# Kernel optimization log

Hardware: AMD Instinct MI355X
Metric: run time of the kernel (lower is better)

## Reference

```python
import jax, jax.numpy as jnp
import numpy as np

N_A = 50000
N_B = 50000
E = 800000
C_IN = 128
C_OUT = 128


def _lstm_cell_seq1(x, W_ih, b):
    # PyTorch LSTM with seq_len=1 and zero initial state: h = o*tanh(i*g)
    # gate order in weight_ih: [i, f, g, o]; f-gate is unused since c0 = 0.
    gates = x @ W_ih.T + b  # [N, 4H]
    i, f, g, o = jnp.split(gates, 4, axis=-1)
    c = jax.nn.sigmoid(i) * jnp.tanh(g)
    return jax.nn.sigmoid(o) * jnp.tanh(c)


def _conv(x_src, x_dst, edge_index, W_ih, b_lstm, W_lin, b_lin):
    # LSTM message depends only on src features -> compute per node, gather per edge.
    msg = _lstm_cell_seq1(x_src, W_ih, b_lstm)          # [N_src, C_OUT]
    src, dst = edge_index[0], edge_index[1]
    aggr = jax.ops.segment_sum(msg[src], dst, num_segments=x_dst.shape[0])  # [N_dst, C_OUT]
    h = jnp.concatenate([x_dst, aggr], axis=-1)          # [N_dst, C_IN + C_OUT]
    return jax.nn.relu(h @ W_lin.T + b_lin)              # dropout = identity (eval mode)


def setup_inputs() -> dict:
    key = jax.random.key(0)
    ks = jax.random.split(key, 12)
    s = 0.05
    return {
        "x_a": jax.random.normal(ks[0], (N_A, C_IN), jnp.float32),
        "x_b": jax.random.normal(ks[1], (N_B, C_IN), jnp.float32),
        "edge_ab": jax.random.randint(ks[2], (2, E), 0, 50000, jnp.int64 if jax.config.jax_enable_x64 else jnp.int32),
        "edge_ba": jax.random.randint(ks[3], (2, E), 0, 50000, jnp.int64 if jax.config.jax_enable_x64 else jnp.int32),
        "W_ih_ab": jax.random.normal(ks[4], (4 * C_OUT, C_IN), jnp.float32) * s,
        "b_ab": jax.random.normal(ks[5], (4 * C_OUT,), jnp.float32) * s,
        "W_lin_ab": jax.random.normal(ks[6], (C_OUT, C_IN + C_OUT), jnp.float32) * s,
        "b_lin_ab": jax.random.normal(ks[7], (C_OUT,), jnp.float32) * s,
        "W_ih_ba": jax.random.normal(ks[8], (4 * C_OUT, C_IN), jnp.float32) * s,
        "b_ba": jax.random.normal(ks[9], (4 * C_OUT,), jnp.float32) * s,
        "W_lin_ba": jax.random.normal(ks[10], (C_OUT, C_IN + C_OUT), jnp.float32) * s,
        "b_lin_ba": jax.random.normal(ks[11], (C_OUT,), jnp.float32) * s,
    }


def reference(x_a, x_b, edge_ab, edge_ba,
              W_ih_ab, b_ab, W_lin_ab, b_lin_ab,
              W_ih_ba, b_ba, W_lin_ba, b_lin_ba):
    # a_to_b relation updates type_b nodes; b_to_a updates type_a nodes.
    out_b = _conv(x_a, x_b, edge_ab, W_ih_ab, b_ab, W_lin_ab, b_lin_ab)
    out_a = _conv(x_b, x_a, edge_ba, W_ih_ba, b_ba, W_lin_ba, b_lin_ba)
    # stack (same shapes) => [2, N, C_OUT]: index 0 = new x_a, index 1 = new x_b
    return jnp.stack([out_a, out_b], axis=0)
```

## Files before the change

kernel.cpp:

```cpp
#include <hip/hip_runtime.h>
#include <cstdint>
#include <cstddef>

#define CCH 128
#define TK 4096
#define FCAP 2560
#define SLOT 2560
#define MAXBKT 1024
#define XPAD 136
#define APAD 264

typedef __attribute__((ext_vector_type(8))) short short8;
typedef __attribute__((ext_vector_type(4))) float floatx4;

__device__ __forceinline__ unsigned short f2bf(float f) {
    unsigned u = __builtin_bit_cast(unsigned, f);
    u += 0x7fffu + ((u >> 16) & 1u);
    return (unsigned short)(u >> 16);
}
__device__ __forceinline__ float bf2f(unsigned short h) {
    unsigned u = ((unsigned)h) << 16;
    return __builtin_bit_cast(float, u);
}
__device__ __forceinline__ float sigmoidf_(float x) { return 1.0f / (1.0f + __expf(-x)); }
__device__ __forceinline__ float tanh_fast(float x) {
    x = fminf(fmaxf(x, -10.0f), 10.0f);
    float e = __expf(2.0f * x);
    return (e - 1.0f) / (e + 1.0f);
}

__global__ __launch_bounds__(256) void prep_weights_kernel(
    const float* __restrict__ Wih0, const float* __restrict__ Wih1,
    const float* __restrict__ Wlin0, const float* __restrict__ Wlin1,
    unsigned short* __restrict__ frag_ih, unsigned short* __restrict__ frag_lin,
    int* __restrict__ btot, int NBKT)
{
    int t = blockIdx.x * 256 + threadIdx.x;
    if (t < 12288) {
        int l  = t & 63;
        int kc = (t >> 6) & 3;
        int ct = (t >> 8) & 7;
        int g  = (t >> 11) % 3;
        int rel = t / 6144;
        int gb = (g == 0) ? 0 : (g == 1 ? 256 : 384);
        const float* W = rel ? Wih1 : Wih0;
        int n  = gb + ct * 16 + (l & 15);
        int kb = kc * 32 + (l >> 4) * 8;
        unsigned short* o = frag_ih + (size_t)t * 8;
#pragma unroll
        for (int j = 0; j < 8; j++) o[j] = f2bf(W[(size_t)n * CCH + kb + j]);
    } else if (t < 20480) {
        int t2 = t - 12288;
        int l  = t2 & 63;
        int kc = (t2 >> 6) & 7;
        int ct = (t2 >> 9) & 7;
        int rel = t2 >> 12;
        const float* W = rel ? Wlin1 : Wlin0;
        int n  = ct * 16 + (l & 15);
        int kb = kc * 32 + (l >> 4) * 8;
        unsigned short* o = frag_lin + (size_t)t2 * 8;
#pragma unroll
        for (int j = 0; j < 8; j++) o[j] = f2bf(W[(size_t)n * 256 + kb + j]);
    } else {
        int z = t - 20480;
        if (z < NBKT) btot[z] = 0;
    }
}

__global__ __launch_bounds__(256) void lstm_scatter_kernel(
    const float* __restrict__ x0, const float* __restrict__ x1,
    const unsigned short* __restrict__ wfrag,
    const float* __restrict__ b0, const float* __restrict__ b1,
    unsigned short* __restrict__ msg0, unsigned short* __restrict__ msg1,
    int N0, int N1, int nblk0,
    const int* __restrict__ src0, const int* __restrict__ dst0,
    const int* __restrict__ src1, const int* __restrict__ dst1,
    int* __restrict__ btot, unsigned* __restrict__ packed,
    int E0, int E1, int nbkt0, int NBKT, int nT)
{
    __shared__ unsigned short xs[32 * XPAD];
    __shared__ int h[MAXBKT];
    __shared__ int cur[MAXBKT];
    const int tid = threadIdx.x;

    if (blockIdx.x < nT) {
        for (int i = tid; i < NBKT; i += 256) h[i] = 0;
        __syncthreads();
        const long long Etot = (long long)E0 + E1;
        const long long base = (long long)blockIdx.x * TK;
        int gg[16];
        unsigned pk[16];
#pragma unroll
        for (int j = 0; j < 16; j++) {
            long long e = base + j * 256 + tid;
            gg[j] = -1;
            if (e < Etot) {
                int s, d, g;
                if (e < E0) { d = dst0[e]; s = src0[e]; g = d >> 7; }
                else { long long ee = e - E0; d = dst1[ee]; s = src1[ee]; g = nbkt0 + (d >> 7); }
                gg[j] = g;
                pk[j] = ((unsigned)(d & 127) << 24) | (unsigned)s;
                atomicAdd(&h[g], 1);
            }
        }
        __syncthreads();
        for (int i = tid; i < NBKT; i += 256) {
            int c = h[i];
            cur[i] = i * SLOT + (c ? atomicAdd(&btot[i], c) : 0);
        }
        __syncthreads();
#pragma unroll
        for (int j = 0; j < 16; j++) {
            if (gg[j] >= 0) {
                int pos = atomicAdd(&cur[gg[j]], 1);
                packed[pos] = pk[j];
            }
        }
        return;
    }

    const int lb = blockIdx.x - nT;
    const int rel = (lb >= nblk0);
    const int nb = (rel ? (lb - nblk0) : lb) * 32;
    const float* x = rel ? x1 : x0;
    const float* bias = rel ? b1 : b0;
    unsigned short* msg = rel ? msg1 : msg0;
    const int N = rel ? N1 : N0;
    const unsigned short* wf = wfrag + (size_t)rel * 6144 * 8;

    {
        int r = tid >> 3;
        int c0 = (tid & 7) * 16;
        int n = nb + r;
        unsigned short* dstp = xs + r * XPAD + c0;
        if (n < N) {
            const float4* srcp = (const float4*)(x + (size_t)n * CCH + c0);
#pragma unroll
            for (int qq = 0; qq < 4; qq++) {
                float4 v = srcp[qq];
                unsigned u0 = (unsigned)f2bf(v.x) | ((unsigned)f2bf(v.y) << 16);
                unsigned u1 = (unsigned)f2bf(v.z) | ((unsigned)f2bf(v.w) << 16);
                *(uint2*)(dstp + qq * 4) = make_uint2(u0, u1);
            }
        } else {
#pragma unroll
            for (int qq = 0; qq < 4; qq++) *(uint2*)(dstp + qq * 4) = make_uint2(0u, 0u);
        }
    }
    __syncthreads();

    const int w = tid >> 6;
    const int l = tid & 63;
    const int ctb2 = w * 2;
    const int q = l >> 4;
    const int m16 = l & 15;

    floatx4 acc[3][2][2];
#pragma unroll
    for (int g = 0; g < 3; g++)
#pragma unroll
        for (int c = 0; c < 2; c++)
#pragma unroll
            for (int mt = 0; mt < 2; mt++) acc[g][c][mt] = (floatx4){0.f, 0.f, 0.f, 0.f};

    const unsigned short* arow0 = xs + m16 * XPAD + q * 8;
    const unsigned short* arow1 = xs + (16 + m16) * XPAD + q * 8;
#pragma unroll
    for (int kc = 0; kc < 4; kc++) {
        short8 af0 = *(const short8*)(arow0 + kc * 32);
        short8 af1 = *(const short8*)(arow1 + kc * 32);
#pragma unroll
        for (int g = 0; g < 3; g++)
#pragma unroll
            for (int c = 0; c < 2; c++) {
                const unsigned short* bp = wf + ((((size_t)g * 8 + (ctb2 + c)) * 4 + kc) * 64 + l) * 8;
                short8 bv = *(const short8*)bp;
                acc[g][c][0] = __builtin_amdgcn_mfma_f32_16x16x32_bf16(af0, bv, acc[g][c][0], 0, 0, 0);
                acc[g][c][1] = __builtin_amdgcn_mfma_f32_16x16x32_bf16(af1, bv, acc[g][c][1], 0, 0, 0);
            }
    }

    __syncthreads();
#pragma unroll
    for (int c = 0; c < 2; c++) {
        const int col = (ctb2 + c) * 16 + m16;
        const float bi = bias[col], bg = bias[256 + col], bo = bias[384 + col];
#pragma unroll
        for (int mt = 0; mt < 2; mt++)
#pragma unroll
            for (int r = 0; r < 4; r++) {
                const int nl = mt * 16 + q * 4 + r;
                float iv = sigmoidf_(acc[0][c][mt][r] + bi);
                float gv = tanh_fast(acc[1][c][mt][r] + bg);
                float ov = sigmoidf_(acc[2][c][mt][r] + bo);
                xs[nl * XPAD + col] = f2bf(ov * tanh_fast(iv * gv));
            }
    }
    __syncthreads();
    {
        int r = tid >> 3;
        int c0 = (tid & 7) * 16;
        int n = nb + r;
        if (n < N) {
            const unsigned short* srow = xs + r * XPAD + c0;
            uint4 v0 = *(const uint4*)(srow);
            uint4 v1 = *(const uint4*)(srow + 8);
            unsigned short* drow = msg + (size_t)n * CCH + c0;
            *(uint4*)(drow) = v0;
            *(uint4*)(drow + 8) = v1;
        }
    }
}

__global__ __launch_bounds__(512) void fine_sort_kernel(
    unsigned* __restrict__ packed, const int* __restrict__ btot,
    int* __restrict__ offs0, int* __restrict__ deg0,
    int* __restrict__ offs1, int* __restrict__ deg1,
    int N0, int N1, int nbkt0)
{
    __shared__ unsigned pin[FCAP];
    __shared__ int hist[128], scn[128], cur[128];
    const int g = blockIdx.x;
    const int tid = threadIdx.x;
    const int base = g * SLOT;
    const int cnt = min(btot[g], FCAP);

    for (int i = tid; i < cnt; i += 512) pin[i] = packed[base + i];
    if (tid < 128) hist[tid] = 0;
    __syncthreads();
    for (int i = tid; i < cnt; i += 512) atomicAdd(&hist[pin[i] >> 24], 1);
    __syncthreads();
    int v = (tid < 128) ? hist[tid] : 0;
    if (tid < 128) scn[tid] = v;
    __syncthreads();
    for (int off = 1; off < 128; off <<= 1) {
        int t = (tid >= off && tid < 128) ? scn[tid - off] : 0;
        __syncthreads();
        if (tid < 128) scn[tid] += t;
        __syncthreads();
    }
    if (tid < 128) {
        int excl = scn[tid] - v;
        cur[tid] = excl;
        const int rel = (g >= nbkt0);
        const int lb = rel ? g - nbkt0 : g;
        const int n = lb * 128 + tid;
        const int N = rel ? N1 : N0;
        if (n < N) {
            if (rel) { offs1[n] = base + excl; deg1[n] = v; }
            else     { offs0[n] = base + excl; deg0[n] = v; }
        }
    }
    __syncthreads();
    int* op = (int*)packed;
    for (int i = tid; i < cnt; i += 512) {
        unsigned p = pin[i];
        int pos = atomicAdd(&cur[p >> 24], 1);
        op[base + pos] = (int)(p & 0x00FFFFFFu);
    }
}

__global__ __launch_bounds__(512) void gather_linear_kernel(
    const float* __restrict__ xd0, const float* __restrict__ xd1,
    const unsigned short* __restrict__ msg0, const unsigned short* __restrict__ msg1,
    const int* __restrict__ csr,
    const int* __restrict__ offs0, const int* __restrict__ offs1,
    const int* __restrict__ deg0, const int* __restrict__ deg1,
    const unsigned short* __restrict__ wfrag,
    const float* __restrict__ bl0, const float* __restrict__ bl1,
    float* __restrict__ out0, float* __restrict__ out1,
    int P0, int P1, int N0, int N1)
{
    __shared__ unsigned short s[32 * APAD];
    const int tid = threadIdx.x;
    const int grp = blockIdx.x >> 3;
    const int sub = blockIdx.x & 7;
    const int rel = (sub >> 2) & 1;
    const int lb = grp * 4 + (sub & 3);
    const int P = rel ? P1 : P0;
    if (lb >= P) return;
    const int nb = lb * 32;
    const float* xd = rel ? xd1 : xd0;
    const unsigned short* msg = rel ? msg1 : msg0;
    const int* offs = rel ? offs1 : offs0;
    const int* deg = rel ? deg1 : deg0;
    const float* bl = rel ? bl1 : bl0;
    float* outp = rel ? out1 : out0;
    const int N = rel ? N1 : N0;
    const unsigned short* wf = wfrag + (size_t)rel * 4096 * 8;

    {
        int r = tid >> 4;
        int c0 = (tid & 15) * 8;
        int n = nb + r;
        unsigned short* drow = s + r * APAD + c0;
        if (n < N) {
            const floatx4* srcp = (const floatx4*)(xd + (size_t)n * CCH + c0);
            floatx4 v0 = __builtin_nontemporal_load(srcp);
            floatx4 v1 = __builtin_nontemporal_load(srcp + 1);
            uint4 u;
            u.x = (unsigned)f2bf(v0[0]) | ((unsigned)f2bf(v0[1]) << 16);
            u.y = (unsigned)f2bf(v0[2]) | ((unsigned)f2bf(v0[3]) << 16);
            u.z = (unsigned)f2bf(v1[0]) | ((unsigned)f2bf(v1[1]) << 16);
            u.w = (unsigned)f2bf(v1[2]) | ((unsigned)f2bf(v1[3]) << 16);
            *(uint4*)drow = u;
        } else {
            *(uint4*)drow = make_uint4(0u, 0u, 0u, 0u);
        }
    }
    {
        const int w = tid >> 6;
        const int l = tid & 63;
        const int g = l >> 4;
        const int c = l & 15;
        const int nloc = w * 4 + g;
        const int n = nb + nloc;
        float a0 = 0.f, a1 = 0.f, a2 = 0.f, a3 = 0.f;
        float a4 = 0.f, a5 = 0.f, a6 = 0.f, a7 = 0.f;
        if (n < N) {
            const int start = offs[n];
            const int cnt = deg[n];
            const int* ce = csr + start;
            const unsigned short* mb = msg + c * 8;
#define ACC8(U) { \
            a0 += bf2f((unsigned short)(U.x)); a1 += bf2f((unsigned short)((U.x) >> 16)); \
            a2 += bf2f((unsigned short)(U.y)); a3 += bf2f((unsigned short)((U.y) >> 16)); \
            a4 += bf2f((unsigned short)(U.z)); a5 += bf2f((unsigned short)((U.z) >> 16)); \
            a6 += bf2f((unsigned short)(U.w)); a7 += bf2f((unsigned short)((U.w) >> 16)); }
            int j = 0;
            if (cnt >= 4) {
                int s0 = ce[0], s1 = ce[1], s2 = ce[2], s3 = ce[3];
                for (; j + 8 <= cnt; j += 4) {
                    uint4 u0 = *(const uint4*)(mb + (size_t)s0 * CCH);
                    uint4 u1 = *(const uint4*)(mb + (size_t)s1 * CCH);
                    uint4 u2 = *(const uint4*)(mb + (size_t)s2 * CCH);
                    uint4 u3 = *(const uint4*)(mb + (size_t)s3 * CCH);
                    s0 = ce[j + 4]; s1 = ce[j + 5]; s2 = ce[j + 6]; s3 = ce[j + 7];
                    ACC8(u0); ACC8(u1); ACC8(u2); ACC8(u3);
                }
                uint4 u0 = *(const uint4*)(mb + (size_t)s0 * CCH);
                uint4 u1 = *(const uint4*)(mb + (size_t)s1 * CCH);
                uint4 u2 = *(const uint4*)(mb + (size_t)s2 * CCH);
                uint4 u3 = *(const uint4*)(mb + (size_t)s3 * CCH);
                ACC8(u0); ACC8(u1); ACC8(u2); ACC8(u3);
                j += 4;
            }
            for (; j < cnt; j++) {
                uint4 u0 = *(const uint4*)(mb + (size_t)ce[j] * CCH);
                ACC8(u0);
            }
#undef ACC8
        }
        uint4 o;
        o.x = (unsigned)f2bf(a0) | ((unsigned)f2bf(a1) << 16);
        o.y = (unsigned)f2bf(a2) | ((unsigned)f2bf(a3) << 16);
        o.z = (unsigned)f2bf(a4) | ((unsigned)f2bf(a5) << 16);
        o.w = (unsigned)f2bf(a6) | ((unsigned)f2bf(a7) << 16);
        *(uint4*)(s + nloc * APAD + CCH + c * 8) = o;
    }
    __syncthreads();

    const int w = tid >> 6;
    const int l = tid & 63;
    const int q = l >> 4;
    const int m16 = l & 15;

    floatx4 acc[2];
    acc[0] = (floatx4){0.f, 0.f, 0.f, 0.f};
    acc[1] = (floatx4){0.f, 0.f, 0.f, 0.f};

    const unsigned short* arow0 = s + m16 * APAD + q * 8;
    const unsigned short* arow1 = s + (16 + m16) * APAD + q * 8;
#pragma unroll
    for (int kc = 0; kc < 8; kc++) {
        short8 af0 = *(const short8*)(arow0 + kc * 32);
        short8 af1 = *(const short8*)(arow1 + kc * 32);
        const unsigned short* bp = wf + ((((size_t)w) * 8 + kc) * 64 + l) * 8;
        short8 bv = *(const short8*)bp;
        acc[0] = __builtin_amdgcn_mfma_f32_16x16x32_bf16(af0, bv, acc[0], 0, 0, 0);
        acc[1] = __builtin_amdgcn_mfma_f32_16x16x32_bf16(af1, bv, acc[1], 0, 0, 0);
    }

    const int col = w * 16 + m16;
    const float bv = bl[col];
#pragma unroll
    for (int mt = 0; mt < 2; mt++)
#pragma unroll
        for (int r = 0; r < 4; r++) {
            const int node = nb + mt * 16 + q * 4 + r;
            if (node < N) {
                float v = fmaxf(acc[mt][r] + bv, 0.0f);
                __builtin_nontemporal_store(v, &outp[(size_t)node * CCH + col]);
            }
        }
}

extern "C" void kernel_launch(void* const* d_in, const int* in_sizes, int n_in,
                              void* d_out, int out_size, void* d_ws, size_t ws_size,
                              hipStream_t stream) {
    const float* x_a      = (const float*)d_in[0];
    const float* x_b      = (const float*)d_in[1];
    const int*   e_ab     = (const int*)d_in[2];
    const int*   e_ba     = (const int*)d_in[3];
    const float* W_ih_ab  = (const float*)d_in[4];
    const float* b_ab     = (const float*)d_in[5];
    const float* W_lin_ab = (const float*)d_in[6];
    const float* b_lin_ab = (const float*)d_in[7];
    const float* W_ih_ba  = (const float*)d_in[8];
    const float* b_ba     = (const float*)d_in[9];
    const float* W_lin_ba = (const float*)d_in[10];
    const float* b_lin_ba = (const float*)d_in[11];

    const int NA = in_sizes[0] / CCH;
    const int NB = in_sizes[1] / CCH;
    const int E0 = in_sizes[2] / 2;
    const int E1 = in_sizes[3] / 2;

    float* out = (float*)d_out;
    char* ws = (char*)d_ws;
    size_t off = 0;
    auto alloc = [&](size_t bytes) { char* p = ws + off; off += (bytes + 255) & ~(size_t)255; return p; };

    unsigned short* wfrag_ih  = (unsigned short*)alloc(12288 * 8 * 2);
    unsigned short* wfrag_lin = (unsigned short*)alloc(8192 * 8 * 2);
    unsigned short* msg_a     = (unsigned short*)alloc((size_t)NA * CCH * 2);
    unsigned short* msg_b     = (unsigned short*)alloc((size_t)NB * CCH * 2);

    const int nbkt0 = (NB + 127) / 128;
    const int nbkt1 = (NA + 127) / 128;
    const int NBKT = nbkt0 + nbkt1;
    const long long Etot = (long long)E0 + E1;
    const int nT = (int)((Etot + TK - 1) / TK);

    int* btot   = (int*)alloc((size_t)NBKT * 4);
    int* offs_b = (int*)alloc((size_t)NB * 4);
    int* offs_a = (int*)alloc((size_t)NA * 4);
    int* deg_b  = (int*)alloc((size_t)NB * 4);
    int* deg_a  = (int*)alloc((size_t)NA * 4);
    unsigned* packed = (unsigned*)alloc((size_t)(NBKT + 1) * SLOT * 4);

    const int nblkA = (NA + 31) / 32;
    const int nblkB = (NB + 31) / 32;

    const int prepG = 80 + (NBKT + 255) / 256;
    prep_weights_kernel<<<prepG, 256, 0, stream>>>(
        W_ih_ab, W_ih_ba, W_lin_ab, W_lin_ba, wfrag_ih, wfrag_lin, btot, NBKT);

    lstm_scatter_kernel<<<nT + nblkA + nblkB, 256, 0, stream>>>(
        x_a, x_b, wfrag_ih, b_ab, b_ba, msg_a, msg_b, NA, NB, nblkA,
        e_ab, e_ab + E0, e_ba, e_ba + E1, btot, packed, E0, E1, nbkt0, NBKT, nT);

    fine_sort_kernel<<<NBKT, 512, 0, stream>>>(
        packed, btot, offs_b, deg_b, offs_a, deg_a, NB, NA, nbkt0);

    const int Pmax = (nblkB > nblkA) ? nblkB : nblkA;
    const int G = ((Pmax + 3) / 4) * 8;
    gather_linear_kernel<<<G, 512, 0, stream>>>(
        x_b, x_a, msg_a, msg_b, (const int*)packed,
        offs_b, offs_a, deg_b, deg_a, wfrag_lin, b_lin_ab, b_lin_ba,
        out + (size_t)NA * CCH, out, nblkB, nblkA, NB, NA);
}
```

Measured before the change: 235.9 us.

## Fuse bucket fine-sort into gather-linear kernel using shared-memory CSR

Merges the per-bucket fine sort and the gather+linear kernels into one kernel: each block sorts its 128-node bucket into shared memory and then processes four 32-node tiles, reading neighbour lists from LDS instead of global CSR/offset/degree arrays. This removes a kernel launch and the global round trip of the sorted CSR and offset/degree arrays. In exchange, each block uses much more LDS (about 37 KB), which lowers occupancy. The grid also drops to roughly 782 large blocks that run four serialized gather/MFMA phases, which reduces parallelism and latency hiding for the random gathers.

```diff
diff --git a/kernel.cpp b/kernel.cpp
--- a/kernel.cpp
+++ b/kernel.cpp
@@ -212,187 +212,159 @@
     }
 }
 
-__global__ __launch_bounds__(512) void fine_sort_kernel(
-    unsigned* __restrict__ packed, const int* __restrict__ btot,
-    int* __restrict__ offs0, int* __restrict__ deg0,
-    int* __restrict__ offs1, int* __restrict__ deg1,
+__global__ __launch_bounds__(512) void sort_gather_linear_kernel(
+    const float* __restrict__ xd0, const float* __restrict__ xd1,
+    const unsigned short* __restrict__ msg0, const unsigned short* __restrict__ msg1,
+    const unsigned* __restrict__ packed, const int* __restrict__ btot,
+    const unsigned short* __restrict__ wfrag,
+    const float* __restrict__ bl0, const float* __restrict__ bl1,
+    float* __restrict__ out0, float* __restrict__ out1,
     int N0, int N1, int nbkt0)
 {
     __shared__ unsigned pin[FCAP];
-    __shared__ int hist[128], scn[128], cur[128];
+    __shared__ int sout_s[FCAP];
+    __shared__ int hist[128], scn[128], cur[128], ndoff[128];
+    __shared__ unsigned short s[32 * APAD];
+
+    const int tid = threadIdx.x;
     const int g = blockIdx.x;
-    const int tid = threadIdx.x;
-    const int base = g * SLOT;
-    const int cnt = min(btot[g], FCAP);
-
-    for (int i = tid; i < cnt; i += 512) pin[i] = packed[base + i];
-    if (tid < 128) hist[tid] = 0;
-    __syncthreads();
-    for (int i = tid; i < cnt; i += 512) atomicAdd(&hist[pin[i] >> 24], 1);
-    __syncthreads();
-    int v = (tid < 128) ? hist[tid] : 0;
-    if (tid < 128) scn[tid] = v;
-    __syncthreads();
-    for (int off = 1; off < 128; off <<= 1) {
-        int t = (tid >= off && tid < 128) ? scn[tid - off] : 0;
-        __syncthreads();
-        if (tid < 128) scn[tid] += t;
-        __syncthreads();
-    }
-    if (tid < 128) {
-        int excl = scn[tid] - v;
-        cur[tid] = excl;
-        const int rel = (g >= nbkt0);
-        const int lb = rel ? g - nbkt0 : g;
-        const int n = lb * 128 + tid;
-        const int N = rel ? N1 : N0;
-        if (n < N) {
-            if (rel) { offs1[n] = base + excl; deg1[n] = v; }
-            else     { offs0[n] = base + excl; deg0[n] = v; }
-        }
-    }
-    __syncthreads();
-    int* op = (int*)packed;
-    for (int i = tid; i < cnt; i += 512) {
-        unsigned p = pin[i];
-        int pos = atomicAdd(&cur[p >> 24], 1);
-        op[base + pos] = (int)(p & 0x00FFFFFFu);
-    }
-}
-
-__global__ __launch_bounds__(512) void gather_linear_kernel(
-    const float* __restrict__ xd0, const float* __restrict__ xd1,
-    const unsigned short* __restrict__ msg0, const unsigned short* __restrict__ msg1,
-    const int* __restrict__ csr,
-    const int* __restrict__ offs0, const int* __restrict__ offs1,
-    const int* __restrict__ deg0, const int* __restrict__ deg1,
-    const unsigned short* __restrict__ wfrag,
-    const float* __restrict__ bl0, const float* __restrict__ bl1,
-    float* __restrict__ out0, float* __restrict__ out1,
-    int P0, int P1, int N0, int N1)
-{
-    __shared__ unsigned short s[32 * APAD];
-    const int tid = threadIdx.x;
-    const int grp = blockIdx.x >> 3;
-    const int sub = blockIdx.x & 7;
-    const int rel = (sub >> 2) & 1;
-    const int lb = grp * 4 + (sub & 3);
-    const int P = rel ? P1 : P0;
-    if (lb >= P) return;
-    const int nb = lb * 32;
+    const int rel = (g >= nbkt0);
+    const int lb = rel ? g - nbkt0 : g;
     const float* xd = rel ? xd1 : xd0;
     const unsigned short* msg = rel ? msg1 : msg0;
-    const int* offs = rel ? offs1 : offs0;
-    const int* deg = rel ? deg1 : deg0;
     const float* bl = rel ? bl1 : bl0;
     float* outp = rel ? out1 : out0;
     const int N = rel ? N1 : N0;
     const unsigned short* wf = wfrag + (size_t)rel * 4096 * 8;
 
-    {
-        int r = tid >> 4;
-        int c0 = (tid & 15) * 8;
-        int n = nb + r;
-        unsigned short* drow = s + r * APAD + c0;
-        if (n < N) {
-            const floatx4* srcp = (const floatx4*)(xd + (size_t)n * CCH + c0);
-            floatx4 v0 = __builtin_nontemporal_load(srcp);
-            floatx4 v1 = __builtin_nontemporal_load(srcp + 1);
-            uint4 u;
-            u.x = (unsigned)f2bf(v0[0]) | ((unsigned)f2bf(v0[1]) << 16);
-            u.y = (unsigned)f2bf(v0[2]) | ((unsigned)f2bf(v0[3]) << 16);
-            u.z = (unsigned)f2bf(v1[0]) | ((unsigned)f2bf(v1[1]) << 16);
-            u.w = (unsigned)f2bf(v1[2]) | ((unsigned)f2bf(v1[3]) << 16);
-            *(uint4*)drow = u;
-        } else {
-            *(uint4*)drow = make_uint4(0u, 0u, 0u, 0u);
-        }
-    }
-    {
-        const int w = tid >> 6;
-        const int l = tid & 63;
-        const int g = l >> 4;
-        const int c = l & 15;
-        const int nloc = w * 4 + g;
-        const int n = nb + nloc;
-        float a0 = 0.f, a1 = 0.f, a2 = 0.f, a3 = 0.f;
-        float a4 = 0.f, a5 = 0.f, a6 = 0.f, a7 = 0.f;
-        if (n < N) {
-            const int start = offs[n];
-            const int cnt = deg[n];
-            const int* ce = csr + start;
-            const unsigned short* mb = msg + c * 8;
+    const int base = g * SLOT;
+    const int cnt = min(btot[g], FCAP);
+
+    for (int i = tid; i < cnt; i += 512) pin[i] = packed[base + i];
+    if (tid < 128) hist[tid] = 0;
+    __syncthreads();
+    for (int i = tid; i < cnt; i += 512) atomicAdd(&hist[pin[i] >> 24], 1);
+    __syncthreads();
+    int v = (tid < 128) ? hist[tid] : 0;
+    if (tid < 128) scn[tid] = v;
+    __syncthreads();
+    for (int off = 1; off < 128; off <<= 1) {
+        int t = (tid >= off && tid < 128) ? scn[tid - off] : 0;
+        __syncthreads();
+        if (tid < 128) scn[tid] += t;
+        __syncthreads();
+    }
+    if (tid < 128) {
+        int excl = scn[tid] - v;
+        cur[tid] = excl;
+        ndoff[tid] = excl;
+    }
+    __syncthreads();
+    for (int i = tid; i < cnt; i += 512) {
+        unsigned p = pin[i];
+        int pos = atomicAdd(&cur[p >> 24], 1);
+        sout_s[pos] = (int)(p & 0x00FFFFFFu);
+    }
+    __syncthreads();
+
+    const int w = tid >> 6;
+    const int l = tid & 63;
+    for (int it = 0; it < 4; ++it) {
+        const int nb = lb * 128 + it * 32;
+
+        {
+            int r = tid >> 4;
+            int c0 = (tid & 15) * 8;
+            int n = nb + r;
+            unsigned short* drow = s + r * APAD + c0;
+            if (n < N) {
+                const floatx4* srcp = (const floatx4*)(xd + (size_t)n * CCH + c0);
+                floatx4 v0 = __builtin_nontemporal_load(srcp);
+                floatx4 v1 = __builtin_nontemporal_load(srcp + 1);
+                uint4 u;
+                u.x = (unsigned)f2bf(v0[0]) | ((unsigned)f2bf(v0[1]) << 16);
+                u.y = (unsigned)f2bf(v0[2]) | ((unsigned)f2bf(v0[3]) << 16);
+                u.z = (unsigned)f2bf(v1[0]) | ((unsigned)f2bf(v1[1]) << 16);
+                u.w = (unsigned)f2bf(v1[2]) | ((unsigned)f2bf(v1[3]) << 16);
+                *(uint4*)drow = u;
+            } else {
+                *(uint4*)drow = make_uint4(0u, 0u, 0u, 0u);
+            }
+        }
+        {
+            const int gl = l >> 4;
+            const int c = l & 15;
+            const int nloc = w * 4 + gl;
+            const int q128 = it * 32 + nloc;
+            const int n = nb + nloc;
+            float a0 = 0.f, a1 = 0.f, a2 = 0.f, a3 = 0.f;
+            float a4 = 0.f, a5 = 0.f, a6 = 0.f, a7 = 0.f;
+            if (n < N) {
+                const int cntn = hist[q128];
+                const int* ce = sout_s + ndoff[q128];
+                const unsigned short* mb = msg + c * 8;
 #define ACC8(U) { \
-            a0 += bf2f((unsigned short)(U.x)); a1 += bf2f((unsigned short)((U.x) >> 16)); \
-            a2 += bf2f((unsigned short)(U.y)); a3 += bf2f((unsigned short)((U.y) >> 16)); \
-            a4 += bf2f((unsigned short)(U.z)); a5 += bf2f((unsigned short)((U.z) >> 16)); \
-            a6 += bf2f((unsigned short)(U.w)); a7 += bf2f((unsigned short)((U.w) >> 16)); }
-            int j = 0;
-            if (cnt >= 4) {
-                int s0 = ce[0], s1 = ce[1], s2 = ce[2], s3 = ce[3];
-                for (; j + 8 <= cnt; j += 4) {
+                a0 += bf2f((unsigned short)(U.x)); a1 += bf2f((unsigned short)((U.x) >> 16)); \
+                a2 += bf2f((unsigned short)(U.y)); a3 += bf2f((unsigned short)((U.y) >> 16)); \
+                a4 += bf2f((unsigned short)(U.z)); a5 += bf2f((unsigned short)((U.z) >> 16)); \
+                a6 += bf2f((unsigned short)(U.w)); a7 += bf2f((unsigned short)((U.w) >> 16)); }
+                int j = 0;
+                for (; j + 4 <= cntn; j += 4) {
+                    int s0 = ce[j], s1 = ce[j + 1], s2 = ce[j + 2], s3 = ce[j + 3];
                     uint4 u0 = *(const uint4*)(mb + (size_t)s0 * CCH);
                     uint4 u1 = *(const uint4*)(mb + (size_t)s1 * CCH);
                     uint4 u2 = *(const uint4*)(mb + (size_t)s2 * CCH);
                     uint4 u3 = *(const uint4*)(mb + (size_t)s3 * CCH);
-                    s0 = ce[j + 4]; s1 = ce[j + 5]; s2 = ce[j + 6]; s3 = ce[j + 7];
                     ACC8(u0); ACC8(u1); ACC8(u2); ACC8(u3);
                 }
-                uint4 u0 = *(const uint4*)(mb + (size_t)s0 * CCH);
-                uint4 u1 = *(const uint4*)(mb + (size_t)s1 * CCH);
-                uint4 u2 = *(const uint4*)(mb + (size_t)s2 * CCH);
-                uint4 u3 = *(const uint4*)(mb + (size_t)s3 * CCH);
-                ACC8(u0); ACC8(u1); ACC8(u2); ACC8(u3);
-                j += 4;
-            }
-            for (; j < cnt; j++) {
-                uint4 u0 = *(const uint4*)(mb + (size_t)ce[j] * CCH);
-                ACC8(u0);
-            }
+                for (; j < cntn; j++) {
+                    uint4 u0 = *(const uint4*)(mb + (size_t)ce[j] * CCH);
+                    ACC8(u0);
+                }
 #undef ACC8
-        }
-        uint4 o;
-        o.x = (unsigned)f2bf(a0) | ((unsigned)f2bf(a1) << 16);
-        o.y = (unsigned)f2bf(a2) | ((unsigned)f2bf(a3) << 16);
-        o.z = (unsigned)f2bf(a4) | ((unsigned)f2bf(a5) << 16);
-        o.w = (unsigned)f2bf(a6) | ((unsigned)f2bf(a7) << 16);
-        *(uint4*)(s + nloc * APAD + CCH + c * 8) = o;
-    }
-    __syncthreads();
-
-    const int w = tid >> 6;
-    const int l = tid & 63;
-    const int q = l >> 4;
-    const int m16 = l & 15;
-
-    floatx4 acc[2];
-    acc[0] = (floatx4){0.f, 0.f, 0.f, 0.f};
-    acc[1] = (floatx4){0.f, 0.f, 0.f, 0.f};
-
-    const unsigned short* arow0 = s + m16 * APAD + q * 8;
-    const unsigned short* arow1 = s + (16 + m16) * APAD + q * 8;
-#pragma unroll
-    for (int kc = 0; kc < 8; kc++) {
-        short8 af0 = *(const short8*)(arow0 + kc * 32);
-        short8 af1 = *(const short8*)(arow1 + kc * 32);
-        const unsigned short* bp = wf + ((((size_t)w) * 8 + kc) * 64 + l) * 8;
-        short8 bv = *(const short8*)bp;
-        acc[0] = __builtin_amdgcn_mfma_f32_16x16x32_bf16(af0, bv, acc[0], 0, 0, 0);
-        acc[1] = __builtin_amdgcn_mfma_f32_16x16x32_bf16(af1, bv, acc[1], 0, 0, 0);
-    }
-
-    const int col = w * 16 + m16;
-    const float bv = bl[col];
-#pragma unroll
-    for (int mt = 0; mt < 2; mt++)
-#pragma unroll
-        for (int r = 0; r < 4; r++) {
-            const int node = nb + mt * 16 + q * 4 + r;
-            if (node < N) {
-                float v = fmaxf(acc[mt][r] + bv, 0.0f);
-                __builtin_nontemporal_store(v, &outp[(size_t)node * CCH + col]);
-            }
-        }
+            }
+            uint4 o;
+            o.x = (unsigned)f2bf(a0) | ((unsigned)f2bf(a1) << 16);
+            o.y = (unsigned)f2bf(a2) | ((unsigned)f2bf(a3) << 16);
+            o.z = (unsigned)f2bf(a4) | ((unsigned)f2bf(a5) << 16);
+            o.w = (unsigned)f2bf(a6) | ((unsigned)f2bf(a7) << 16);
+            *(uint4*)(s + nloc * APAD + CCH + c * 8) = o;
+        }
+        __syncthreads();
+
+        const int q = l >> 4;
+        const int m16 = l & 15;
+
+        floatx4 acc[2];
+        acc[0] = (floatx4){0.f, 0.f, 0.f, 0.f};
+        acc[1] = (floatx4){0.f, 0.f, 0.f, 0.f};
+
+        const unsigned short* arow0 = s + m16 * APAD + q * 8;
+        const unsigned short* arow1 = s + (16 + m16) * APAD + q * 8;
+#pragma unroll
+        for (int kc = 0; kc < 8; kc++) {
+            short8 af0 = *(const short8*)(arow0 + kc * 32);
+            short8 af1 = *(const short8*)(arow1 + kc * 32);
+            const unsigned short* bp = wf + ((((size_t)w) * 8 + kc) * 64 + l) * 8;
+            short8 bv = *(const short8*)bp;
+            acc[0] = __builtin_amdgcn_mfma_f32_16x16x32_bf16(af0, bv, acc[0], 0, 0, 0);
+            acc[1] = __builtin_amdgcn_mfma_f32_16x16x32_bf16(af1, bv, acc[1], 0, 0, 0);
+        }
+
+        const int col = w * 16 + m16;
+        const float bv = bl[col];
+#pragma unroll
+        for (int mt = 0; mt < 2; mt++)
+#pragma unroll
+            for (int r = 0; r < 4; r++) {
+                const int node = nb + mt * 16 + q * 4 + r;
+                if (node < N) {
+                    float vo = fmaxf(acc[mt][r] + bv, 0.0f);
+                    __builtin_nontemporal_store(vo, &outp[(size_t)node * CCH + col]);
+                }
+            }
+        __syncthreads();
+    }
 }
 
 extern "C" void kernel_launch(void* const* d_in, const int* in_sizes, int n_in,
@@ -433,10 +405,6 @@
     const int nT = (int)((Etot + TK - 1) / TK);
 
     int* btot   = (int*)alloc((size_t)NBKT * 4);
-    int* offs_b = (int*)alloc((size_t)NB * 4);
-    int* offs_a = (int*)alloc((size_t)NA * 4);
-    int* deg_b  = (int*)alloc((size_t)NB * 4);
-    int* deg_a  = (int*)alloc((size_t)NA * 4);
     unsigned* packed = (unsigned*)alloc((size_t)(NBKT + 1) * SLOT * 4);
 
     const int nblkA = (NA + 31) / 32;
@@ -450,13 +418,7 @@
         x_a, x_b, wfrag_ih, b_ab, b_ba, msg_a, msg_b, NA, NB, nblkA,
         e_ab, e_ab + E0, e_ba, e_ba + E1, btot, packed, E0, E1, nbkt0, NBKT, nT);
 
-    fine_sort_kernel<<<NBKT, 512, 0, stream>>>(
-        packed, btot, offs_b, deg_b, offs_a, deg_a, NB, NA, nbkt0);
-
-    const int Pmax = (nblkB > nblkA) ? nblkB : nblkA;
-    const int G = ((Pmax + 3) / 4) * 8;
-    gather_linear_kernel<<<G, 512, 0, stream>>>(
-        x_b, x_a, msg_a, msg_b, (const int*)packed,
-        offs_b, offs_a, deg_b, deg_a, wfrag_lin, b_lin_ab, b_lin_ba,
-        out + (size_t)NA * CCH, out, nblkB, nblkA, NB, NA);
-}
+    sort_gather_linear_kernel<<<NBKT, 512, 0, stream>>>(
+        x_b, x_a, msg_a, msg_b, packed, btot, wfrag_lin,
+        b_lin_ab, b_lin_ba, out + (size_t)NA * CCH, out, NB, NA, nbkt0);
+}
```

New measurement: 244.6 us. 3.7% more time.
